# Performance work log

Hardware: AMD Instinct MI355X
Metric: run time of the kernel (lower is better)

Reference implementation:

```python
import jax, jax.numpy as jnp
import numpy as np

NUM_HEADS = 12
THETA = 10000.0


def _rope(x, pos):
    # x: [B, H, S, dk]; interleaved even/odd pair rotation
    dk = x.shape[-1]
    freqs = THETA ** (-jnp.arange(dk // 2, dtype=jnp.float32) * 2.0 / dk)  # [dk/2]
    ang = pos.astype(jnp.float32)[:, None] * freqs                         # [S, dk/2]
    cos, sin = jnp.cos(ang), jnp.sin(ang)
    x1, x2 = x[..., 0::2], x[..., 1::2]
    rot = jnp.stack([x1 * cos - x2 * sin, x1 * sin + x2 * cos], axis=-1)
    return rot.reshape(x.shape)


def setup_inputs() -> dict:
    key = jax.random.key(0)
    ks = jax.random.split(key, 5)
    B, S, D = 4, 2048, 768
    w_scale = 1.0 / np.sqrt(D).astype(np.float32)
    x = jax.random.normal(ks[0], (B, S, D), dtype=jnp.float32)
    Wq = jax.random.normal(ks[1], (D, D), dtype=jnp.float32) * w_scale
    Wk = jax.random.normal(ks[2], (D, D), dtype=jnp.float32) * w_scale
    Wv = jax.random.normal(ks[3], (D, D), dtype=jnp.float32) * w_scale
    Wo = jax.random.normal(ks[4], (D, D), dtype=jnp.float32) * w_scale
    token_positions = jnp.arange(S, dtype=jnp.int32)
    return {"x": x, "Wq": Wq, "Wk": Wk, "Wv": Wv, "Wo": Wo,
            "token_positions": token_positions}


def reference(x, Wq, Wk, Wv, Wo, token_positions):
    B, S, D = x.shape
    H = NUM_HEADS
    dk = D // H
    # bias-free linear layers: y = x @ W^T (torch Linear weight convention)
    q = (x @ Wq.T).reshape(B, S, H, dk).transpose(0, 2, 1, 3)  # [B,H,S,dk]
    k = (x @ Wk.T).reshape(B, S, H, dk).transpose(0, 2, 1, 3)
    v = (x @ Wv.T).reshape(B, S, H, dk).transpose(0, 2, 1, 3)
    q = _rope(q, token_positions)
    k = _rope(k, token_positions)
    scores = jnp.einsum('bhqd,bhkd->bhqk', q, k) / np.float32(np.sqrt(dk))
    causal = jnp.tril(jnp.ones((S, S), dtype=bool))
    scores = jnp.where(causal, scores, -jnp.inf)
    attn = jax.nn.softmax(scores, axis=-1)                      # [B,H,S,S]
    out = jnp.einsum('bhqk,bhkd->bhqd', attn, v)
    out = out.transpose(0, 2, 1, 3).reshape(B, S, D)
    return out @ Wo.T
```

## Files before the change

### kernel.cpp

```cpp
#include <hip/hip_runtime.h>
#include <cstdint>
#include <cstddef>

#define NTOK 8192
#define SLEN 2048
#define DM   768
#define NH   12
#define DKH  64

typedef __attribute__((ext_vector_type(8))) short bf16x8;
typedef __attribute__((ext_vector_type(4))) float f32x4;

__device__ __forceinline__ float b2f(unsigned short u) {
  return __uint_as_float(((unsigned)u) << 16);
}
__device__ __forceinline__ unsigned short f2b(float f) {
  unsigned u = __float_as_uint(f);
  u += 0x7fffu + ((u >> 16) & 1u);
  return (unsigned short)(u >> 16);
}
__device__ __forceinline__ unsigned cvtpk(float lo, float hi) {
  unsigned r;
  asm("v_cvt_pk_bf16_f32 %0, %1, %2" : "=v"(r) : "v"(lo), "v"(hi));
  return r;
}

__device__ __forceinline__ void gld16(const void* g, void* l) {
  __builtin_amdgcn_global_load_lds(
      (const __attribute__((address_space(1))) void*)g,
      (__attribute__((address_space(3))) void*)l, 16, 0, 0);
}

#define BAR_DRAIN() do {                                  \
    asm volatile("s_waitcnt vmcnt(0)" ::: "memory");      \
    __builtin_amdgcn_s_barrier();                         \
    __builtin_amdgcn_sched_barrier(0);                    \
  } while (0)

__global__ void cast_all_kernel(const float* __restrict__ x,
                                const float* __restrict__ w0,
                                const float* __restrict__ w1,
                                const float* __restrict__ w2,
                                const float* __restrict__ w3,
                                unsigned short* __restrict__ xb,
                                unsigned short* __restrict__ wb) {
  const int bid = blockIdx.x, tid = threadIdx.x;
  const float* src;
  unsigned short* dst;
  size_t i;
  if (bid < 3072) {
    src = x; dst = xb; i = (size_t)bid * 256 + tid;
  } else {
    const int wbid = bid - 3072;
    const int w = wbid / 288;
    src = (w == 0) ? w0 : (w == 1) ? w1 : (w == 2) ? w2 : w3;
    dst = wb + (size_t)w * DM * DM;
    i = (size_t)(wbid - w * 288) * 256 + tid;
  }
  const float4* p = (const float4*)(src + i * 8);
  float4 a = p[0], b = p[1];
  union { unsigned short h[8]; bf16x8 v; } u;
  u.h[0] = f2b(a.x); u.h[1] = f2b(a.y); u.h[2] = f2b(a.z); u.h[3] = f2b(a.w);
  u.h[4] = f2b(b.x); u.h[5] = f2b(b.y); u.h[6] = f2b(b.z); u.h[7] = f2b(b.w);
  *(bf16x8*)(dst + i * 8) = u.v;
}

__global__ __launch_bounds__(256, 3) void gemm_qkv_kernel(
    const unsigned short* __restrict__ A, const unsigned short* __restrict__ Ball,
    unsigned short* __restrict__ Qb, unsigned short* __restrict__ Kb,
    unsigned short* __restrict__ VTout,
    const int* __restrict__ pos) {
  const int K = DM;
  const int tid = threadIdx.x, wid = tid >> 6, lane = tid & 63;
  const int lrow = lane & 15, g = lane >> 4, lk8 = g * 8;
  const int m0 = blockIdx.y * 64, n0 = blockIdx.x * 128;
  const int wm = (wid >> 1) * 32, wn = (wid & 1) * 64;
  const int sr = wid * 8 + (lane >> 3), sc = (lane & 7) * 8;
  const int ssw = sc ^ ((sr & 7) << 3);
  __shared__ unsigned short At[64 * 64];
  __shared__ unsigned short Bt[128 * 64];
  f32x4 acc[2][4] = {};

  const unsigned short* ap = A    + (size_t)(m0 + sr) * K + ssw;
  const unsigned short* bp = Ball + (size_t)(n0 + sr) * K + ssw;

  int aoff[2][2], boff[2][4];
#pragma unroll
  for (int ks = 0; ks < 2; ++ks) {
#pragma unroll
    for (int mi = 0; mi < 2; ++mi) {
      int ra = wm + mi * 16 + lrow;
      aoff[ks][mi] = (ra * 64 + ((ks * 32 + lk8) ^ ((ra & 7) << 3))) * 2;
    }
#pragma unroll
    for (int ni = 0; ni < 4; ++ni) {
      int rb = wn + ni * 16 + lrow;
      boff[ks][ni] = (rb * 64 + ((ks * 32 + lk8) ^ ((rb & 7) << 3))) * 2;
    }
  }
  const char* Atc = (const char*)At;
  const char* Btc = (const char*)Bt;

  const int nk = K >> 6;
  for (int kk = 0; kk < nk; ++kk) {
    __syncthreads();
    gld16(ap,          &At[(wid * 8) * 64]);
    gld16(ap + 32 * K, &At[(32 + wid * 8) * 64]);
#pragma unroll
    for (int rnd = 0; rnd < 4; ++rnd)
      gld16(bp + rnd * 32 * K, &Bt[(rnd * 32 + wid * 8) * 64]);
    ap += 64; bp += 64;
    __syncthreads();
    bf16x8 af[2][2], bfr[2][4];
#pragma unroll
    for (int ks = 0; ks < 2; ++ks) {
#pragma unroll
      for (int mi = 0; mi < 2; ++mi)
        af[ks][mi] = *(const bf16x8*)(Atc + aoff[ks][mi]);
#pragma unroll
      for (int ni = 0; ni < 4; ++ni)
        bfr[ks][ni] = *(const bf16x8*)(Btc + boff[ks][ni]);
    }
#pragma unroll
    for (int ks = 0; ks < 2; ++ks)
#pragma unroll
      for (int mi = 0; mi < 2; ++mi)
#pragma unroll
        for (int ni = 0; ni < 4; ++ni)
          acc[mi][ni] = __builtin_amdgcn_mfma_f32_16x16x32_bf16(
              bfr[ks][ni], af[ks][mi], acc[mi][ni], 0, 0, 0);
  }

  const int nsec = blockIdx.x / 6;
  const int nn0 = n0 - nsec * 768;

  if (nsec == 2) {
#pragma unroll
    for (int mi = 0; mi < 2; ++mi) {
      const int m = m0 + wm + mi * 16 + lrow;
      const int bb = m >> 11, st = m & (SLEN - 1);
      const int scol = (st & ~63) | (st & 35) |
                       (((st >> 4) & 1) << 2) | (((st >> 2) & 1) << 3) |
                       (((st >> 3) & 1) << 4);
#pragma unroll
      for (int ni = 0; ni < 4; ++ni) {
        const int nb = nn0 + wn + ni * 16 + g * 4;
        const int hh = nb >> 6, dd = nb & 63;
        unsigned short* dst =
            VTout + ((size_t)(bb * NH + hh) * DKH + dd) * SLEN + scol;
#pragma unroll
        for (int r = 0; r < 4; ++r)
          dst[(size_t)r * SLEN] = f2b(acc[mi][ni][r]);
      }
    }
    return;
  }

  unsigned short* Cp = (nsec == 0) ? Qb : Kb;
  float frq[4][2];
#pragma unroll
  for (int ni = 0; ni < 4; ++ni)
#pragma unroll
    for (int rp = 0; rp < 2; ++rp)
      frq[ni][rp] = exp2f(
          (float)(((wn + ni * 16 + g * 4 + rp * 2) & 63) >> 1) *
          -0.4152410118609203f);
#pragma unroll
  for (int mi = 0; mi < 2; ++mi) {
    const int m = m0 + wm + mi * 16 + lrow;
    const float ps = (float)pos[m & (SLEN - 1)];
#pragma unroll
    for (int ni = 0; ni < 4; ++ni) {
#pragma unroll
      for (int rp = 0; rp < 2; ++rp) {
        float sn, cs;
        __sincosf(ps * frq[ni][rp], &sn, &cs);
        float x1 = acc[mi][ni][2 * rp], x2 = acc[mi][ni][2 * rp + 1];
        acc[mi][ni][2 * rp]     = fmaf(x1, cs, -x2 * sn);
        acc[mi][ni][2 * rp + 1] = fmaf(x1, sn, x2 * cs);
      }
      union { unsigned u[2]; ushort4 s; } o;
      o.u[0] = cvtpk(acc[mi][ni][0], acc[mi][ni][1]);
      o.u[1] = cvtpk(acc[mi][ni][2], acc[mi][ni][3]);
      *(ushort4*)&Cp[(size_t)m * DM + nn0 + wn + ni * 16 + g * 4] = o.s;
    }
  }
}

__global__ __launch_bounds__(256, 3) void gemm_out_kernel(
    const unsigned short* __restrict__ A, const unsigned short* __restrict__ B,
    float* __restrict__ C) {
  const int K = DM, N = DM;
  const int tid = threadIdx.x, wid = tid >> 6, lane = tid & 63;
  const int lrow = lane & 15, g = lane >> 4, lk8 = g * 8;
  const int m0 = blockIdx.y * 64, n0 = blockIdx.x * 128;
  const int wm = (wid >> 1) * 32, wn = (wid & 1) * 64;
  const int sr = wid * 8 + (lane >> 3), sc = (lane & 7) * 8;
  const int ssw = sc ^ ((sr & 7) << 3);
  __shared__ unsigned short At[64 * 64];
  __shared__ unsigned short Bt[128 * 64];
  f32x4 acc[2][4] = {};

  const unsigned short* ap = A + (size_t)(m0 + sr) * K + ssw;
  const unsigned short* bp = B + (size_t)(n0 + sr) * K + ssw;

  int aoff[2][2], boff[2][4];
#pragma unroll
  for (int ks = 0; ks < 2; ++ks) {
#pragma unroll
    for (int mi = 0; mi < 2; ++mi) {
      int ra = wm + mi * 16 + lrow;
      aoff[ks][mi] = (ra * 64 + ((ks * 32 + lk8) ^ ((ra & 7) << 3))) * 2;
    }
#pragma unroll
    for (int ni = 0; ni < 4; ++ni) {
      int rb = wn + ni * 16 + lrow;
      boff[ks][ni] = (rb * 64 + ((ks * 32 + lk8) ^ ((rb & 7) << 3))) * 2;
    }
  }
  const char* Atc = (const char*)At;
  const char* Btc = (const char*)Bt;

  const int nk = K >> 6;
  for (int kk = 0; kk < nk; ++kk) {
    __syncthreads();
    gld16(ap,          &At[(wid * 8) * 64]);
    gld16(ap + 32 * K, &At[(32 + wid * 8) * 64]);
#pragma unroll
    for (int rnd = 0; rnd < 4; ++rnd)
      gld16(bp + rnd * 32 * K, &Bt[(rnd * 32 + wid * 8) * 64]);
    ap += 64; bp += 64;
    __syncthreads();
    bf16x8 af[2][2], bfr[2][4];
#pragma unroll
    for (int ks = 0; ks < 2; ++ks) {
#pragma unroll
      for (int mi = 0; mi < 2; ++mi)
        af[ks][mi] = *(const bf16x8*)(Atc + aoff[ks][mi]);
#pragma unroll
      for (int ni = 0; ni < 4; ++ni)
        bfr[ks][ni] = *(const bf16x8*)(Btc + boff[ks][ni]);
    }
#pragma unroll
    for (int ks = 0; ks < 2; ++ks)
#pragma unroll
      for (int mi = 0; mi < 2; ++mi)
#pragma unroll
        for (int ni = 0; ni < 4; ++ni)
          acc[mi][ni] = __builtin_amdgcn_mfma_f32_16x16x32_bf16(
              bfr[ks][ni], af[ks][mi], acc[mi][ni], 0, 0, 0);
  }

#pragma unroll
  for (int mi = 0; mi < 2; ++mi) {
    const int m = m0 + wm + mi * 16 + lrow;
#pragma unroll
    for (int ni = 0; ni < 4; ++ni)
      *(f32x4*)&C[(size_t)m * N + n0 + wn + ni * 16 + g * 4] = acc[mi][ni];
  }
}

__global__ __launch_bounds__(256, 4) void attn_kernel(
    const unsigned short* __restrict__ Q, const unsigned short* __restrict__ Kg,
    const unsigned short* __restrict__ VT, unsigned short* __restrict__ O) {
  const int bh = blockIdx.x;
  const int s = 31 - (int)blockIdx.y;
  const int nt = s + 1;
  const int b = bh / NH, h = bh - b * NH;
  const size_t base = ((size_t)b * SLEN) * DM + h * DKH;
  const size_t vbase = (size_t)bh * DKH * SLEN;
  const int tid = threadIdx.x, wid = tid >> 6, lane = tid & 63;
  const int lrow = lane & 15, g = lane >> 4;
  const int rloc = wid * 16 + lrow;

  __shared__ unsigned short Kt[2][64 * 64];
  __shared__ unsigned short Vt[2][64 * 64];

  bf16x8 qf[2];
#pragma unroll
  for (int ks = 0; ks < 2; ++ks) {
    union { unsigned short h[8]; bf16x8 v; } u;
    u.v = *(const bf16x8*)&Q[base + (size_t)(s * 64 + rloc) * DM + ks * 32 + g * 8];
#pragma unroll
    for (int j = 0; j < 8; ++j)
      u.h[j] = f2b(b2f(u.h[j]) * 0.18033688011112042f);
    qf[ks] = u.v;
  }

  union { unsigned short h[8]; bf16x8 v; } one_u;
#pragma unroll
  for (int j = 0; j < 8; ++j) one_u.h[j] = 0x3F80;
  const bf16x8 ones = one_u.v;

  f32x4 oacc[4] = {};
  f32x4 l_acc = {};

  const int srow = wid * 8 + (lane >> 3);
  const int ssw = ((lane & 7) * 8) ^ ((srow & 7) << 3);
  const unsigned short* kp = Kg + base + (size_t)srow * DM + ssw;
  const unsigned short* vp = VT + vbase + (size_t)srow * SLEN + ssw;

  int roff[2][4];
#pragma unroll
  for (int ks = 0; ks < 2; ++ks)
#pragma unroll
    for (int ni = 0; ni < 4; ++ni) {
      int rr = ni * 16 + lrow;
      roff[ks][ni] = (rr * 64 + ((ks * 32 + g * 8) ^ ((rr & 7) << 3))) * 2;
    }

  auto stage = [&](int buf) {
    gld16(kp,             &Kt[buf][(wid * 8) * 64]);
    gld16(kp + 32 * DM,   &Kt[buf][(32 + wid * 8) * 64]);
    gld16(vp,             &Vt[buf][(wid * 8) * 64]);
    gld16(vp + 32 * SLEN, &Vt[buf][(32 + wid * 8) * 64]);
    kp += 64 * DM;
    vp += 64;
  };

  auto compute = [&](int t, int buf) {
    const char* Ksb = (const char*)&Kt[buf][0];
    const char* Vsb = (const char*)&Vt[buf][0];

    f32x4 sa[4] = {};
    __builtin_amdgcn_s_setprio(1);
#pragma unroll
    for (int ks = 0; ks < 2; ++ks)
#pragma unroll
      for (int ni = 0; ni < 4; ++ni) {
        bf16x8 kf = *(const bf16x8*)(Ksb + roff[ks][ni]);
        sa[ni] = __builtin_amdgcn_mfma_f32_16x16x32_bf16(
            kf, qf[ks], sa[ni], 0, 0, 0);
      }
    __builtin_amdgcn_s_setprio(0);

    if (t == s) {
#pragma unroll
      for (int ni = 0; ni < 4; ++ni)
#pragma unroll
        for (int r = 0; r < 4; ++r)
          if (ni * 16 + g * 4 + r > rloc) sa[ni][r] = -1e30f;
    }

#pragma unroll
    for (int ni = 0; ni < 4; ++ni)
#pragma unroll
      for (int r = 0; r < 4; ++r)
        sa[ni][r] = exp2f(sa[ni][r]);

    bf16x8 pf[2];
#pragma unroll
    for (int ks = 0; ks < 2; ++ks) {
      union { unsigned u[4]; bf16x8 v; } uu;
      uu.u[0] = cvtpk(sa[2 * ks][0],     sa[2 * ks][1]);
      uu.u[1] = cvtpk(sa[2 * ks][2],     sa[2 * ks][3]);
      uu.u[2] = cvtpk(sa[2 * ks + 1][0], sa[2 * ks + 1][1]);
      uu.u[3] = cvtpk(sa[2 * ks + 1][2], sa[2 * ks + 1][3]);
      pf[ks] = uu.v;
    }

    __builtin_amdgcn_s_setprio(1);
#pragma unroll
    for (int ks = 0; ks < 2; ++ks) {
#pragma unroll
      for (int ni = 0; ni < 4; ++ni) {
        bf16x8 vf = *(const bf16x8*)(Vsb + roff[ks][ni]);
        oacc[ni] = __builtin_amdgcn_mfma_f32_16x16x32_bf16(
            vf, pf[ks], oacc[ni], 0, 0, 0);
      }
      l_acc = __builtin_amdgcn_mfma_f32_16x16x32_bf16(
          ones, pf[ks], l_acc, 0, 0, 0);
    }
    __builtin_amdgcn_s_setprio(0);
  };

  stage(0);
  BAR_DRAIN();
  int cur = 0;
  for (int t = 0; t < nt; ++t) {
    if (t + 1 < nt) stage(cur ^ 1);
    compute(t, cur);
    BAR_DRAIN();
    cur ^= 1;
  }

  const float inv = 1.f / l_acc[0];
  const int qrow = s * 64 + rloc;
#pragma unroll
  for (int ni = 0; ni < 4; ++ni) {
    union { unsigned u[2]; ushort4 s4; } o;
    o.u[0] = cvtpk(oacc[ni][0] * inv, oacc[ni][1] * inv);
    o.u[1] = cvtpk(oacc[ni][2] * inv, oacc[ni][3] * inv);
    *(ushort4*)&O[base + (size_t)qrow * DM + ni * 16 + g * 4] = o.s4;
  }
}

extern "C" void kernel_launch(void* const* d_in, const int* in_sizes, int n_in,
                              void* d_out, int out_size, void* d_ws, size_t ws_size,
                              hipStream_t stream) {
  const float* x  = (const float*)d_in[0];
  const float* Wq = (const float*)d_in[1];
  const float* Wk = (const float*)d_in[2];
  const float* Wv = (const float*)d_in[3];
  const float* Wo = (const float*)d_in[4];
  const int* pos  = (const int*)d_in[5];
  float* out = (float*)d_out;

  char* ws = (char*)d_ws;
  size_t off = 0;
  auto carve = [&](size_t bytes) -> void* {
    void* p = ws + off;
    off += (bytes + 255) & ~(size_t)255;
    return p;
  };
  unsigned short* xb  = (unsigned short*)carve((size_t)NTOK * DM * 2);
  unsigned short* wqb = (unsigned short*)carve((size_t)DM * DM * 2 * 4);
  unsigned short* wob = wqb + (size_t)3 * DM * DM;
  unsigned short* Qb  = (unsigned short*)carve((size_t)NTOK * DM * 2);
  unsigned short* Kb  = (unsigned short*)carve((size_t)NTOK * DM * 2);
  unsigned short* Ab  = (unsigned short*)carve((size_t)NTOK * DM * 2);
  unsigned short* VTb = (unsigned short*)carve((size_t)4 * NH * DKH * SLEN * 2);

  cast_all_kernel<<<dim3(3072 + 4 * 288), dim3(256), 0, stream>>>(
      x, Wq, Wk, Wv, Wo, xb, wqb);

  gemm_qkv_kernel<<<dim3(18, 128), dim3(256), 0, stream>>>(
      xb, wqb, Qb, Kb, VTb, pos);

  attn_kernel<<<dim3(48, 32), dim3(256), 0, stream>>>(Qb, Kb, VTb, Ab);

  gemm_out_kernel<<<dim3(6, 128), dim3(256), 0, stream>>>(Ab, wob, out);
}
```

Before: 117.1 us.

## Double-buffer LDS tiles in QKV and output projection GEMMs

```diff
diff --git a/kernel.cpp b/kernel.cpp
--- a/kernel.cpp
+++ b/kernel.cpp
@@ -77,8 +77,8 @@
   const int wm = (wid >> 1) * 32, wn = (wid & 1) * 64;
   const int sr = wid * 8 + (lane >> 3), sc = (lane & 7) * 8;
   const int ssw = sc ^ ((sr & 7) << 3);
-  __shared__ unsigned short At[64 * 64];
-  __shared__ unsigned short Bt[128 * 64];
+  __shared__ unsigned short At[2][64 * 64];
+  __shared__ unsigned short Bt[2][128 * 64];
   f32x4 acc[2][4] = {};
 
   const unsigned short* ap = A    + (size_t)(m0 + sr) * K + ssw;
@@ -98,19 +98,24 @@
       boff[ks][ni] = (rb * 64 + ((ks * 32 + lk8) ^ ((rb & 7) << 3))) * 2;
     }
   }
-  const char* Atc = (const char*)At;
-  const char* Btc = (const char*)Bt;
+
+  auto stage = [&](int buf) {
+    gld16(ap,          &At[buf][(wid * 8) * 64]);
+    gld16(ap + 32 * K, &At[buf][(32 + wid * 8) * 64]);
+#pragma unroll
+    for (int rnd = 0; rnd < 4; ++rnd)
+      gld16(bp + rnd * 32 * K, &Bt[buf][(rnd * 32 + wid * 8) * 64]);
+    ap += 64; bp += 64;
+  };
 
   const int nk = K >> 6;
+  stage(0);
+  BAR_DRAIN();
   for (int kk = 0; kk < nk; ++kk) {
-    __syncthreads();
-    gld16(ap,          &At[(wid * 8) * 64]);
-    gld16(ap + 32 * K, &At[(32 + wid * 8) * 64]);
-#pragma unroll
-    for (int rnd = 0; rnd < 4; ++rnd)
-      gld16(bp + rnd * 32 * K, &Bt[(rnd * 32 + wid * 8) * 64]);
-    ap += 64; bp += 64;
-    __syncthreads();
+    const int cur = kk & 1;
+    if (kk + 1 < nk) stage(cur ^ 1);
+    const char* Atc = (const char*)&At[cur][0];
+    const char* Btc = (const char*)&Bt[cur][0];
     bf16x8 af[2][2], bfr[2][4];
 #pragma unroll
     for (int ks = 0; ks < 2; ++ks) {
@@ -129,6 +134,7 @@
         for (int ni = 0; ni < 4; ++ni)
           acc[mi][ni] = __builtin_amdgcn_mfma_f32_16x16x32_bf16(
               bfr[ks][ni], af[ks][mi], acc[mi][ni], 0, 0, 0);
+    BAR_DRAIN();
   }
 
   const int nsec = blockIdx.x / 6;
@@ -197,8 +203,8 @@
   const int wm = (wid >> 1) * 32, wn = (wid & 1) * 64;
   const int sr = wid * 8 + (lane >> 3), sc = (lane & 7) * 8;
   const int ssw = sc ^ ((sr & 7) << 3);
-  __shared__ unsigned short At[64 * 64];
-  __shared__ unsigned short Bt[128 * 64];
+  __shared__ unsigned short At[2][64 * 64];
+  __shared__ unsigned short Bt[2][128 * 64];
   f32x4 acc[2][4] = {};
 
   const unsigned short* ap = A + (size_t)(m0 + sr) * K + ssw;
@@ -218,19 +224,24 @@
       boff[ks][ni] = (rb * 64 + ((ks * 32 + lk8) ^ ((rb & 7) << 3))) * 2;
     }
   }
-  const char* Atc = (const char*)At;
-  const char* Btc = (const char*)Bt;
+
+  auto stage = [&](int buf) {
+    gld16(ap,          &At[buf][(wid * 8) * 64]);
+    gld16(ap + 32 * K, &At[buf][(32 + wid * 8) * 64]);
+#pragma unroll
+    for (int rnd = 0; rnd < 4; ++rnd)
+      gld16(bp + rnd * 32 * K, &Bt[buf][(rnd * 32 + wid * 8) * 64]);
+    ap += 64; bp += 64;
+  };
 
   const int nk = K >> 6;
+  stage(0);
+  BAR_DRAIN();
   for (int kk = 0; kk < nk; ++kk) {
-    __syncthreads();
-    gld16(ap,          &At[(wid * 8) * 64]);
-    gld16(ap + 32 * K, &At[(32 + wid * 8) * 64]);
-#pragma unroll
-    for (int rnd = 0; rnd < 4; ++rnd)
-      gld16(bp + rnd * 32 * K, &Bt[(rnd * 32 + wid * 8) * 64]);
-    ap += 64; bp += 64;
-    __syncthreads();
+    const int cur = kk & 1;
+    if (kk + 1 < nk) stage(cur ^ 1);
+    const char* Atc = (const char*)&At[cur][0];
+    const char* Btc = (const char*)&Bt[cur][0];
     bf16x8 af[2][2], bfr[2][4];
 #pragma unroll
     for (int ks = 0; ks < 2; ++ks) {
@@ -249,6 +260,7 @@
         for (int ni = 0; ni < 4; ++ni)
           acc[mi][ni] = __builtin_amdgcn_mfma_f32_16x16x32_bf16(
               bfr[ks][ni], af[ks][mi], acc[mi][ni], 0, 0, 0);
+    BAR_DRAIN();
   }
 
 #pragma unroll
```

New measurement: 125.8 us. +7.5%, slower.
